# Optimization experiments

Hardware: AMD Instinct MI355X
Metric: run time of the kernel (lower is better)

## Reference

```python
import jax, jax.numpy as jnp
import numpy as np

NA = 100000
NB = 100000
E = 500000
D = 256
EPS = 1e-5


def setup_inputs() -> dict:
    key = jax.random.key(0)
    ks = jax.random.split(key, 10)
    scale = 1.0 / np.sqrt(D)
    return {
        "feat_a": jax.random.normal(ks[0], (NA, D), jnp.float32),
        "feat_b": jax.random.normal(ks[1], (NB, D), jnp.float32),
        "src_ab": jax.random.randint(ks[2], (E,), 0, NA, jnp.int32),
        "dst_ab": jax.random.randint(ks[3], (E,), 0, NB, jnp.int32),
        "src_ba": jax.random.randint(ks[4], (E,), 0, NB, jnp.int32),
        "dst_ba": jax.random.randint(ks[5], (E,), 0, NA, jnp.int32),
        "WT_ab": jax.random.normal(ks[6], (D, D), jnp.float32) * scale,
        "WT_ba": jax.random.normal(ks[7], (D, D), jnp.float32) * scale,
        "WA_ab": jax.random.normal(ks[8], (1, D), jnp.float32) * scale,
        "WA_ba": jax.random.normal(ks[9], (1, D), jnp.float32) * scale,
        "gamma": jnp.ones((D,), jnp.float32),
        "beta": jnp.zeros((D,), jnp.float32),
    }


def _etype_agg(h_src, h_dst, src, dst, WT, WA, n_dst):
    # per-etype linear on src nodes: t_h = W_T h_src
    t_h = h_src @ WT.T                              # [Ns, D]
    x = t_h[src] * h_dst[dst]                       # u_mul_v -> [E, D]
    s = jnp.exp(x @ WA.T)                           # exp(W_A x) -> [E, 1]
    att_sum = jax.ops.segment_sum(s, dst, num_segments=n_dst)  # copy_e+sum
    att = s / att_sum[dst]                          # e_div_v (dst of an edge always has >=1 edge)
    # u_mul_e + sum: weighted scatter of raw src features
    return jax.ops.segment_sum(h_src[src] * att, dst, num_segments=n_dst)


def _finalize(h, gamma, beta):
    h = jax.nn.relu(h)
    mu = jnp.mean(h, axis=-1, keepdims=True)
    var = jnp.mean(jnp.square(h - mu), axis=-1, keepdims=True)
    return (h - mu) / jnp.sqrt(var + EPS) * gamma + beta  # dropout is identity (eval)


def reference(feat_a, feat_b, src_ab, dst_ab, src_ba, dst_ba,
              WT_ab, WT_ba, WA_ab, WA_ba, gamma, beta):
    h_b = _etype_agg(feat_a, feat_b, src_ab, dst_ab, WT_ab, WA_ab, NB)
    h_a = _etype_agg(feat_b, feat_a, src_ba, dst_ba, WT_ba, WA_ba, NA)
    out_a = _finalize(h_a, gamma, beta)
    out_b = _finalize(h_b, gamma, beta)
    return jnp.stack([out_a, out_b])  # [2, N, D]
```

## Files before the change

kernel.cpp:

```cpp
#include <hip/hip_runtime.h>
#include <hip/hip_bf16.h>

#define D 256

typedef __attribute__((ext_vector_type(8))) short short8;
typedef __attribute__((ext_vector_type(4))) float f32x4;
typedef __attribute__((ext_vector_type(4))) unsigned short u16x4;

__device__ __forceinline__ unsigned short f2bf(float f) {
  unsigned int u = __builtin_bit_cast(unsigned int, f);
  u = (u + 0x7FFFu + ((u >> 16) & 1u)) >> 16;
  return (unsigned short)u;
}
__device__ __forceinline__ float bf2f(unsigned short h) {
  unsigned int u = ((unsigned int)h) << 16;
  return __builtin_bit_cast(float, u);
}

__global__ void zero_f32(float* __restrict__ p, int n) {
  int i = blockIdx.x * 256 + threadIdx.x;
  if (i < n) p[i] = 0.f;
}
__global__ void zero2_k(int* __restrict__ a, int na, int* __restrict__ b, int nb) {
  int i = blockIdx.x * 256 + threadIdx.x;
  if (i < na) a[i] = 0;
  else if (i - na < nb) b[i - na] = 0;
}

__global__ void classify_k(const float* __restrict__ q0, const float* __restrict__ q1,
                           const float* __restrict__ q2, const float* __restrict__ q3,
                           int* __restrict__ flags) {
  __shared__ int cnt1[4], cnt0[4];
  int t = threadIdx.x;
  if (t < 4) { cnt1[t] = 0; cnt0[t] = 0; }
  __syncthreads();
  const float* qs[4] = {q0, q1, q2, q3};
#pragma unroll
  for (int v = 0; v < 4; ++v) {
    float x = qs[v][t];
    if (x == 1.0f) atomicAdd(&cnt1[v], 1);
    if (x == 0.0f) atomicAdd(&cnt0[v], 1);
  }
  __syncthreads();
  if (t == 0) {
    int gi = -1, bi = -1;
    for (int v = 0; v < 4; ++v) if (cnt1[v] == 256 && gi < 0) gi = v;
    for (int v = 0; v < 4; ++v) if (cnt0[v] == 256 && v != gi && bi < 0) bi = v;
    if (gi < 0) gi = 2;
    if (bi < 0) bi = (gi == 3) ? 2 : 3;
    int wa[2], w = 0;
    for (int v = 0; v < 4; ++v) if (v != gi && v != bi) { if (w < 2) wa[w] = v; ++w; }
    flags[0] = wa[0]; flags[1] = wa[1]; flags[2] = gi; flags[3] = bi;
  }
}

__global__ void prep_w2(const float* __restrict__ WT_ab, const float* __restrict__ WT_ba,
                        const float* __restrict__ q0, const float* __restrict__ q1,
                        const float* __restrict__ q2, const float* __restrict__ q3,
                        const int* __restrict__ flags,
                        unsigned short* __restrict__ w2ab, unsigned short* __restrict__ w2ba) {
  const float* qs[4] = {q0, q1, q2, q3};
  const float* WAab = qs[flags[0]];
  const float* WAba = qs[flags[1]];
  int i = blockIdx.x * 256 + threadIdx.x;
  int n = i >> 8;
  w2ab[i] = f2bf(WAab[n] * WT_ab[i]);
  w2ba[i] = f2bf(WAba[n] * WT_ba[i]);
}

__global__ __launch_bounds__(512) void gemm_g(const float* __restrict__ feat,
                                              const unsigned short* __restrict__ w2,
                                              unsigned short* __restrict__ g,
                                              unsigned short* __restrict__ featbf,
                                              int nchunks, int do_featbf) {
  __shared__ __align__(16) unsigned char bl[2][8192];
  int lane = threadIdx.x & 63;
  int wv = threadIdx.x >> 6;
  int c0 = blockIdx.x * 8 + wv;
  bool active = c0 < nchunks;
  int c = active ? c0 : (nchunks - 1);
  int r16 = lane & 15;
  int kg = lane >> 4;
  int row0 = c * 32;

  short8 a[2][8];
#pragma unroll
  for (int sub = 0; sub < 2; ++sub) {
    int row = row0 + sub * 16 + r16;
    const float* rp = feat + (size_t)row * D + kg * 8;
#pragma unroll
    for (int kk = 0; kk < 8; ++kk) {
      f32x4 x0 = *(const f32x4*)(rp + kk * 32);
      f32x4 x1 = *(const f32x4*)(rp + kk * 32 + 4);
      short8 t;
      t[0] = (short)f2bf(x0[0]); t[1] = (short)f2bf(x0[1]);
      t[2] = (short)f2bf(x0[2]); t[3] = (short)f2bf(x0[3]);
      t[4] = (short)f2bf(x1[0]); t[5] = (short)f2bf(x1[1]);
      t[6] = (short)f2bf(x1[2]); t[7] = (short)f2bf(x1[3]);
      a[sub][kk] = t;
      if (do_featbf && active)
        *(short8*)(featbf + (size_t)row * D + kk * 32 + kg * 8) = t;
    }
  }

  int t = threadIdx.x;
  int brow = t >> 5, bc = t & 31;
  int slin = brow * 512 + bc * 16;
  int sswz = slin ^ ((brow & 7) << 4);

  *(short8*)(bl[0] + sswz) = *(const short8*)(w2 + (size_t)brow * D + bc * 8);
  __syncthreads();

  int cur = 0;
#pragma unroll 1
  for (int nt = 0; nt < 16; ++nt) {
    short8 tnext;
    bool has = nt + 1 < 16;
    if (has)
      tnext = *(const short8*)(w2 + (size_t)((nt + 1) * 16 + brow) * D + bc * 8);

    f32x4 acc0 = {0.f, 0.f, 0.f, 0.f};
    f32x4 acc1 = {0.f, 0.f, 0.f, 0.f};
    const unsigned char* blc = bl[cur];
#pragma unroll
    for (int kk = 0; kk < 8; ++kk) {
      int lin = r16 * 512 + kk * 64 + kg * 16;
      int swz = lin ^ ((r16 & 7) << 4);
      short8 b = *(const short8*)(blc + swz);
      acc0 = __builtin_amdgcn_mfma_f32_16x16x32_bf16(a[0][kk], b, acc0, 0, 0, 0);
      acc1 = __builtin_amdgcn_mfma_f32_16x16x32_bf16(a[1][kk], b, acc1, 0, 0, 0);
    }
    if (active) {
      int colv = nt * 16 + r16;
#pragma unroll
      for (int j = 0; j < 4; ++j) {
        int r = row0 + kg * 4 + j;
        g[(size_t)r * D + colv] = f2bf(acc0[j]);
        g[(size_t)(r + 16) * D + colv] = f2bf(acc1[j]);
      }
    }
    if (has) *(short8*)(bl[cur ^ 1] + sswz) = tnext;
    __syncthreads();
    cur ^= 1;
  }
}

__global__ void hist2_k(const int* __restrict__ dab, int* __restrict__ degb,
                        const int* __restrict__ dba, int* __restrict__ dega, int E) {
  int i = blockIdx.x * blockDim.x + threadIdx.x;
  if (i < E) atomicAdd(&degb[dab[i]], 1);
  else if (i - E < E) atomicAdd(&dega[dba[i - E]], 1);
}

__global__ void scanA2_k(const int* __restrict__ degb, int* __restrict__ rpb,
                         int* __restrict__ bsb, int nB,
                         const int* __restrict__ dega, int* __restrict__ rpa,
                         int* __restrict__ bsa, int nA, int nbB) {
  __shared__ int sh[1024];
  bool isB = (int)blockIdx.x < nbB;
  const int* deg = isB ? degb : dega;
  int* rp = isB ? rpb : rpa;
  int* bsum = isB ? bsb : bsa;
  int n = isB ? nB : nA;
  int blk = isB ? blockIdx.x : blockIdx.x - nbB;
  int i = blk * 1024 + threadIdx.x;
  int v = (i < n) ? deg[i] : 0;
  sh[threadIdx.x] = v;
  __syncthreads();
  for (int off = 1; off < 1024; off <<= 1) {
    int tv = (threadIdx.x >= (unsigned)off) ? sh[threadIdx.x - off] : 0;
    __syncthreads();
    sh[threadIdx.x] += tv;
    __syncthreads();
  }
  if (i < n) rp[i] = sh[threadIdx.x] - v;
  if (threadIdx.x == 1023) bsum[blk] = sh[1023];
}

__global__ void scanB_k(int* __restrict__ bsB, int* __restrict__ bsA, int nbB, int nbA) {
  __shared__ int sh[128];
  int* b = (blockIdx.x == 0) ? bsB : bsA;
  int nb = (blockIdx.x == 0) ? nbB : nbA;
  int t = threadIdx.x;
  int v = (t < nb) ? b[t] : 0;
  sh[t] = v;
  __syncthreads();
  for (int off = 1; off < 128; off <<= 1) {
    int u = (t >= off) ? sh[t - off] : 0;
    __syncthreads();
    sh[t] += u;
    __syncthreads();
  }
  if (t < nb) b[t] = sh[t] - v;
}

__global__ void scanC2_k(int* __restrict__ rpb, int* __restrict__ curb,
                         const int* __restrict__ bsb, int nB,
                         int* __restrict__ rpa, int* __restrict__ cura,
                         const int* __restrict__ bsa, int nA, int nbB, int E) {
  bool isB = (int)blockIdx.x < nbB;
  int* rp = isB ? rpb : rpa;
  int* cursor = isB ? curb : cura;
  const int* bsum = isB ? bsb : bsa;
  int n = isB ? nB : nA;
  int blk = isB ? blockIdx.x : blockIdx.x - nbB;
  int i = blk * 1024 + threadIdx.x;
  if (i < n) {
    int v = rp[i] + bsum[i >> 10];
    rp[i] = v;
    cursor[i] = v;
  }
  if (i == 0) rp[n] = E;
}

__global__ void scatter2_k(const int* __restrict__ sab, const int* __restrict__ dab,
                           int* __restrict__ curb, int* __restrict__ colab,
                           const int* __restrict__ sba, const int* __restrict__ dba,
                           int* __restrict__ cura, int* __restrict__ colba, int E) {
  int i = blockIdx.x * blockDim.x + threadIdx.x;
  if (i < E) {
    int slot = atomicAdd(&curb[dab[i]], 1);
    colab[slot] = sab[i];
  } else if (i - E < E) {
    int j = i - E;
    int slot = atomicAdd(&cura[dba[j]], 1);
    colba[slot] = sba[j];
  }
}

__global__ __launch_bounds__(256) void agg_ln_bf(const unsigned short* __restrict__ fsrc,
                                                 const float* __restrict__ feat_dst,
                                                 const unsigned short* __restrict__ g,
                                                 const int* __restrict__ rp,
                                                 const int* __restrict__ colsrc,
                                                 const float* __restrict__ q0,
                                                 const float* __restrict__ q1,
                                                 const float* __restrict__ q2,
                                                 const float* __restrict__ q3,
                                                 const int* __restrict__ flags,
                                                 float* __restrict__ out, int n_dst) {
  const float* qs[4] = {q0, q1, q2, q3};
  const float* gamma = qs[flags[2]];
  const float* beta  = qs[flags[3]];
  int lane = threadIdx.x & 63;
  int v = blockIdx.x * 4 + (threadIdx.x >> 6);
  if (v >= n_dst) return;
  f32x4 hv = *(const f32x4*)(feat_dst + (size_t)v * D + lane * 4);
  int beg = rp[v], end = rp[v + 1];

  float ssum = 0.f;
  f32x4 acc = {0.f, 0.f, 0.f, 0.f};
  if (beg < end) {
    int last = end - 1;
    int e1 = (beg + 1 <= last) ? beg + 1 : last;
    int e2 = (beg + 2 <= last) ? beg + 2 : last;
    int sc0 = colsrc[beg], sc1 = colsrc[e1], sc2 = colsrc[e2];
    u16x4 gq0 = *(const u16x4*)(g + (size_t)sc0 * D + lane * 4);
    u16x4 fq0 = *(const u16x4*)(fsrc + (size_t)sc0 * D + lane * 4);
    u16x4 gq1 = *(const u16x4*)(g + (size_t)sc1 * D + lane * 4);
    u16x4 fq1 = *(const u16x4*)(fsrc + (size_t)sc1 * D + lane * 4);
    u16x4 gq2 = *(const u16x4*)(g + (size_t)sc2 * D + lane * 4);
    u16x4 fq2 = *(const u16x4*)(fsrc + (size_t)sc2 * D + lane * 4);
    for (int i = beg; i < end; ++i) {
      int ip = (i + 3 <= last) ? i + 3 : last;
      int scn = colsrc[ip];
      u16x4 gqn = *(const u16x4*)(g + (size_t)scn * D + lane * 4);
      u16x4 fqn = *(const u16x4*)(fsrc + (size_t)scn * D + lane * 4);

      float d = bf2f(gq0[0]) * hv[0] + bf2f(gq0[1]) * hv[1] +
                bf2f(gq0[2]) * hv[2] + bf2f(gq0[3]) * hv[3];
#pragma unroll
      for (int off = 32; off > 0; off >>= 1) d += __shfl_xor(d, off, 64);
      float s = __expf(d);
      ssum += s;
      acc[0] += bf2f(fq0[0]) * s; acc[1] += bf2f(fq0[1]) * s;
      acc[2] += bf2f(fq0[2]) * s; acc[3] += bf2f(fq0[3]) * s;

      gq0 = gq1; fq0 = fq1;
      gq1 = gq2; fq1 = fq2;
      gq2 = gqn; fq2 = fqn;
    }
  }
  float inv = (end > beg) ? (1.f / ssum) : 0.f;
  acc[0] *= inv; acc[1] *= inv; acc[2] *= inv; acc[3] *= inv;

  acc[0] = fmaxf(acc[0], 0.f); acc[1] = fmaxf(acc[1], 0.f);
  acc[2] = fmaxf(acc[2], 0.f); acc[3] = fmaxf(acc[3], 0.f);

  float sm = acc[0] + acc[1] + acc[2] + acc[3];
#pragma unroll
  for (int off = 32; off > 0; off >>= 1) sm += __shfl_xor(sm, off, 64);
  float mu = sm * (1.f / 256.f);
  f32x4 dl;
  dl[0] = acc[0] - mu; dl[1] = acc[1] - mu; dl[2] = acc[2] - mu; dl[3] = acc[3] - mu;
  float sq = dl[0] * dl[0] + dl[1] * dl[1] + dl[2] * dl[2] + dl[3] * dl[3];
#pragma unroll
  for (int off = 32; off > 0; off >>= 1) sq += __shfl_xor(sq, off, 64);
  float rs = rsqrtf(sq * (1.f / 256.f) + 1e-5f);

  f32x4 gm = *(const f32x4*)(gamma + lane * 4);
  f32x4 bt = *(const f32x4*)(beta + lane * 4);
  f32x4 o;
  o[0] = dl[0] * rs * gm[0] + bt[0];
  o[1] = dl[1] * rs * gm[1] + bt[1];
  o[2] = dl[2] * rs * gm[2] + bt[2];
  o[3] = dl[3] * rs * gm[3] + bt[3];
  *(f32x4*)(out + (size_t)v * D + lane * 4) = o;
}

__global__ __launch_bounds__(256) void agg_ln(const float* __restrict__ feat_src,
                                              const float* __restrict__ feat_dst,
                                              const unsigned short* __restrict__ g,
                                              const int* __restrict__ rp,
                                              const int* __restrict__ colsrc,
                                              const float* __restrict__ q0,
                                              const float* __restrict__ q1,
                                              const float* __restrict__ q2,
                                              const float* __restrict__ q3,
                                              const int* __restrict__ flags,
                                              float* __restrict__ out, int n_dst) {
  const float* qs[4] = {q0, q1, q2, q3};
  const float* gamma = qs[flags[2]];
  const float* beta  = qs[flags[3]];
  int lane = threadIdx.x & 63;
  int v = blockIdx.x * 4 + (threadIdx.x >> 6);
  if (v >= n_dst) return;
  f32x4 hv = *(const f32x4*)(feat_dst + (size_t)v * D + lane * 4);
  int beg = rp[v], end = rp[v + 1];

  float ssum = 0.f;
  f32x4 acc = {0.f, 0.f, 0.f, 0.f};
  for (int i = beg; i < end; ++i) {
    int sc = colsrc[i];
    u16x4 gq = *(const u16x4*)(g + (size_t)sc * D + lane * 4);
    float d = bf2f(gq[0]) * hv[0] + bf2f(gq[1]) * hv[1] +
              bf2f(gq[2]) * hv[2] + bf2f(gq[3]) * hv[3];
#pragma unroll
    for (int off = 32; off > 0; off >>= 1) d += __shfl_xor(d, off, 64);
    float s = __expf(d);
    ssum += s;
    f32x4 f = *(const f32x4*)(feat_src + (size_t)sc * D + lane * 4);
    acc[0] += f[0] * s; acc[1] += f[1] * s;
    acc[2] += f[2] * s; acc[3] += f[3] * s;
  }
  float inv = (end > beg) ? (1.f / ssum) : 0.f;
  acc[0] *= inv; acc[1] *= inv; acc[2] *= inv; acc[3] *= inv;

  acc[0] = fmaxf(acc[0], 0.f); acc[1] = fmaxf(acc[1], 0.f);
  acc[2] = fmaxf(acc[2], 0.f); acc[3] = fmaxf(acc[3], 0.f);

  float sm = acc[0] + acc[1] + acc[2] + acc[3];
#pragma unroll
  for (int off = 32; off > 0; off >>= 1) sm += __shfl_xor(sm, off, 64);
  float mu = sm * (1.f / 256.f);
  f32x4 dl;
  dl[0] = acc[0] - mu; dl[1] = acc[1] - mu; dl[2] = acc[2] - mu; dl[3] = acc[3] - mu;
  float sq = dl[0] * dl[0] + dl[1] * dl[1] + dl[2] * dl[2] + dl[3] * dl[3];
#pragma unroll
  for (int off = 32; off > 0; off >>= 1) sq += __shfl_xor(sq, off, 64);
  float rs = rsqrtf(sq * (1.f / 256.f) + 1e-5f);

  f32x4 gm = *(const f32x4*)(gamma + lane * 4);
  f32x4 bt = *(const f32x4*)(beta + lane * 4);
  f32x4 o;
  o[0] = dl[0] * rs * gm[0] + bt[0];
  o[1] = dl[1] * rs * gm[1] + bt[1];
  o[2] = dl[2] * rs * gm[2] + bt[2];
  o[3] = dl[3] * rs * gm[3] + bt[3];
  *(f32x4*)(out + (size_t)v * D + lane * 4) = o;
}

extern "C" void kernel_launch(void* const* d_in, const int* in_sizes, int n_in,
                              void* d_out, int out_size, void* d_ws, size_t ws_size,
                              hipStream_t stream) {
  const float* feat_a = (const float*)d_in[0];
  const float* feat_b = (const float*)d_in[1];
  const int* src_ab = (const int*)d_in[2];
  const int* dst_ab = (const int*)d_in[3];
  const int* src_ba = (const int*)d_in[4];
  const int* dst_ba = (const int*)d_in[5];
  const float* WT_ab = (const float*)d_in[6];
  const float* WT_ba = (const float*)d_in[7];
  const float* q0 = (const float*)d_in[8];
  const float* q1 = (const float*)d_in[9];
  const float* q2 = (const float*)d_in[10];
  const float* q3 = (const float*)d_in[11];

  int NA = in_sizes[0] / D;
  int NB = in_sizes[1] / D;
  int E = in_sizes[2];

  float* out = (float*)d_out;
  float* out_a = out;
  float* out_b = out + (size_t)NA * D;

  char* w = (char*)d_ws;
  size_t off = 0;
  auto alloc = [&](size_t bytes) -> void* {
    void* p = (void*)(w + off);
    off += (bytes + 255) & ~(size_t)255;
    return p;
  };
  size_t nmax = (size_t)(NA > NB ? NA : NB);
  unsigned short* gws = (unsigned short*)alloc(nmax * D * 2);
  unsigned short* w2ab = (unsigned short*)alloc(65536 * 2);
  unsigned short* w2ba = (unsigned short*)alloc(65536 * 2);
  int* dc_b = (int*)alloc((size_t)NB * 4);
  int* dc_a = (int*)alloc((size_t)NA * 4);
  int* rp_b = (int*)alloc((size_t)(NB + 1) * 4);
  int* rp_a = (int*)alloc((size_t)(NA + 1) * 4);
  int* col_ab = (int*)alloc((size_t)E * 4);
  int* col_ba = (int*)alloc((size_t)E * 4);
  int* bs_b = (int*)alloc(512);
  int* bs_a = (int*)alloc(512);
  int* flags = (int*)alloc(256);
  size_t need_base = off;
  unsigned short* featbf = (unsigned short*)alloc(nmax * D * 2);
  size_t need_full = off;

  bool bad = (n_in != 12);
  bad = bad || (in_sizes[0] != in_sizes[1]);
  bad = bad || (in_sizes[2] != in_sizes[3]) || (in_sizes[3] != in_sizes[4]) ||
        (in_sizes[4] != in_sizes[5]);
  bad = bad || (in_sizes[6] != 65536) || (in_sizes[7] != 65536);
  bad = bad || (in_sizes[8] != 256) || (in_sizes[9] != 256) ||
        (in_sizes[10] != 256) || (in_sizes[11] != 256);
  bad = bad || (out_size != (NA + NB) * D);
  bad = bad || (ws_size < need_base);
  if (bad) {
    zero_f32<<<(out_size + 255) / 256, 256, 0, stream>>>(out, out_size);
    return;
  }
  int fast = (ws_size >= need_full) ? 1 : 0;

  classify_k<<<1, 256, 0, stream>>>(q0, q1, q2, q3, flags);
  zero2_k<<<(NA + NB + 255) / 256, 256, 0, stream>>>(dc_b, NB, dc_a, NA);
  prep_w2<<<256, 256, 0, stream>>>(WT_ab, WT_ba, q0, q1, q2, q3, flags,
                                   w2ab, w2ba);

  hist2_k<<<(2 * E + 255) / 256, 256, 0, stream>>>(dst_ab, dc_b, dst_ba, dc_a, E);

  int nbB = (NB + 1023) / 1024, nbA = (NA + 1023) / 1024;
  scanA2_k<<<nbB + nbA, 1024, 0, stream>>>(dc_b, rp_b, bs_b, NB,
                                           dc_a, rp_a, bs_a, NA, nbB);
  scanB_k<<<2, 128, 0, stream>>>(bs_b, bs_a, nbB, nbA);
  scanC2_k<<<nbB + nbA, 1024, 0, stream>>>(rp_b, dc_b, bs_b, NB,
                                           rp_a, dc_a, bs_a, NA, nbB, E);
  scatter2_k<<<(2 * E + 255) / 256, 256, 0, stream>>>(src_ab, dst_ab, dc_b, col_ab,
                                                      src_ba, dst_ba, dc_a, col_ba, E);

  int chA = (NA + 31) / 32, chB = (NB + 31) / 32;

  gemm_g<<<(chA + 7) / 8, 512, 0, stream>>>(feat_a, w2ab, gws, featbf, chA, fast);
  if (fast)
    agg_ln_bf<<<(NB + 3) / 4, 256, 0, stream>>>(featbf, feat_b, gws, rp_b, col_ab,
                                                q0, q1, q2, q3, flags, out_b, NB);
  else
    agg_ln<<<(NB + 3) / 4, 256, 0, stream>>>(feat_a, feat_b, gws, rp_b, col_ab,
                                             q0, q1, q2, q3, flags, out_b, NB);

  gemm_g<<<(chB + 7) / 8, 512, 0, stream>>>(feat_b, w2ba, gws, featbf, chB, fast);
  if (fast)
    agg_ln_bf<<<(NA + 3) / 4, 256, 0, stream>>>(featbf, feat_a, gws, rp_a, col_ba,
                                                q0, q1, q2, q3, flags, out_a, NA);
  else
    agg_ln<<<(NA + 3) / 4, 256, 0, stream>>>(feat_b, feat_a, gws, rp_a, col_ba,
                                             q0, q1, q2, q3, flags, out_a, NA);
}
```

Measured before the change: 446.4 us.

## Precompute both bf16 feature copies and read bf16 dst features in aggregation

Adds a workspace buffer so both GEMMs run first. One projected matrix is stored in the unused output half (out_a) as scratch, and each GEMM also emits a bf16 copy of its input features. A new aggregation kernel then reads the destination features in bf16 instead of fp32, and the gather prefetch depth in both aggregation kernels drops from three edges ahead to one. This halves the destination-feature traffic and reduces register pressure. The costs are less latency hiding on the gathers, bf16 rounding of h_dst in the attention dot product, and a dependence on out_a being free until the last kernel overwrites it.

```diff
diff --git a/kernel.cpp b/kernel.cpp
--- a/kernel.cpp
+++ b/kernel.cpp
@@ -228,6 +228,77 @@
   }
 }
 
+__global__ __launch_bounds__(256) void agg_ln_bb(const unsigned short* __restrict__ fsrc,
+                                                 const unsigned short* __restrict__ hdst,
+                                                 const unsigned short* __restrict__ g,
+                                                 const int* __restrict__ rp,
+                                                 const int* __restrict__ colsrc,
+                                                 const float* __restrict__ q0,
+                                                 const float* __restrict__ q1,
+                                                 const float* __restrict__ q2,
+                                                 const float* __restrict__ q3,
+                                                 const int* __restrict__ flags,
+                                                 float* __restrict__ out, int n_dst) {
+  const float* qs[4] = {q0, q1, q2, q3};
+  const float* gamma = qs[flags[2]];
+  const float* beta  = qs[flags[3]];
+  int lane = threadIdx.x & 63;
+  int v = blockIdx.x * 4 + (threadIdx.x >> 6);
+  if (v >= n_dst) return;
+  u16x4 hq = *(const u16x4*)(hdst + (size_t)v * D + lane * 4);
+  f32x4 hv;
+  hv[0] = bf2f(hq[0]); hv[1] = bf2f(hq[1]); hv[2] = bf2f(hq[2]); hv[3] = bf2f(hq[3]);
+  int beg = rp[v], end = rp[v + 1];
+
+  float ssum = 0.f;
+  f32x4 acc = {0.f, 0.f, 0.f, 0.f};
+  if (beg < end) {
+    int sc = colsrc[beg];
+    u16x4 gq = *(const u16x4*)(g + (size_t)sc * D + lane * 4);
+    u16x4 fq = *(const u16x4*)(fsrc + (size_t)sc * D + lane * 4);
+    for (int i = beg; i < end; ++i) {
+      int ip = (i + 1 < end) ? (i + 1) : i;
+      int scn = colsrc[ip];
+      u16x4 gqn = *(const u16x4*)(g + (size_t)scn * D + lane * 4);
+      u16x4 fqn = *(const u16x4*)(fsrc + (size_t)scn * D + lane * 4);
+      float d = bf2f(gq[0]) * hv[0] + bf2f(gq[1]) * hv[1] +
+                bf2f(gq[2]) * hv[2] + bf2f(gq[3]) * hv[3];
+#pragma unroll
+      for (int off = 32; off > 0; off >>= 1) d += __shfl_xor(d, off, 64);
+      float s = __expf(d);
+      ssum += s;
+      acc[0] += bf2f(fq[0]) * s; acc[1] += bf2f(fq[1]) * s;
+      acc[2] += bf2f(fq[2]) * s; acc[3] += bf2f(fq[3]) * s;
+      gq = gqn; fq = fqn;
+    }
+  }
+  float inv = (end > beg) ? (1.f / ssum) : 0.f;
+  acc[0] *= inv; acc[1] *= inv; acc[2] *= inv; acc[3] *= inv;
+
+  acc[0] = fmaxf(acc[0], 0.f); acc[1] = fmaxf(acc[1], 0.f);
+  acc[2] = fmaxf(acc[2], 0.f); acc[3] = fmaxf(acc[3], 0.f);
+
+  float sm = acc[0] + acc[1] + acc[2] + acc[3];
+#pragma unroll
+  for (int off = 32; off > 0; off >>= 1) sm += __shfl_xor(sm, off, 64);
+  float mu = sm * (1.f / 256.f);
+  f32x4 dl;
+  dl[0] = acc[0] - mu; dl[1] = acc[1] - mu; dl[2] = acc[2] - mu; dl[3] = acc[3] - mu;
+  float sq = dl[0] * dl[0] + dl[1] * dl[1] + dl[2] * dl[2] + dl[3] * dl[3];
+#pragma unroll
+  for (int off = 32; off > 0; off >>= 1) sq += __shfl_xor(sq, off, 64);
+  float rs = rsqrtf(sq * (1.f / 256.f) + 1e-5f);
+
+  f32x4 gm = *(const f32x4*)(gamma + lane * 4);
+  f32x4 bt = *(const f32x4*)(beta + lane * 4);
+  f32x4 o;
+  o[0] = dl[0] * rs * gm[0] + bt[0];
+  o[1] = dl[1] * rs * gm[1] + bt[1];
+  o[2] = dl[2] * rs * gm[2] + bt[2];
+  o[3] = dl[3] * rs * gm[3] + bt[3];
+  *(f32x4*)(out + (size_t)v * D + lane * 4) = o;
+}
+
 __global__ __launch_bounds__(256) void agg_ln_bf(const unsigned short* __restrict__ fsrc,
                                                  const float* __restrict__ feat_dst,
                                                  const unsigned short* __restrict__ g,
@@ -251,34 +322,23 @@
   float ssum = 0.f;
   f32x4 acc = {0.f, 0.f, 0.f, 0.f};
   if (beg < end) {
-    int last = end - 1;
-    int e1 = (beg + 1 <= last) ? beg + 1 : last;
-    int e2 = (beg + 2 <= last) ? beg + 2 : last;
-    int sc0 = colsrc[beg], sc1 = colsrc[e1], sc2 = colsrc[e2];
-    u16x4 gq0 = *(const u16x4*)(g + (size_t)sc0 * D + lane * 4);
-    u16x4 fq0 = *(const u16x4*)(fsrc + (size_t)sc0 * D + lane * 4);
-    u16x4 gq1 = *(const u16x4*)(g + (size_t)sc1 * D + lane * 4);
-    u16x4 fq1 = *(const u16x4*)(fsrc + (size_t)sc1 * D + lane * 4);
-    u16x4 gq2 = *(const u16x4*)(g + (size_t)sc2 * D + lane * 4);
-    u16x4 fq2 = *(const u16x4*)(fsrc + (size_t)sc2 * D + lane * 4);
+    int sc = colsrc[beg];
+    u16x4 gq = *(const u16x4*)(g + (size_t)sc * D + lane * 4);
+    u16x4 fq = *(const u16x4*)(fsrc + (size_t)sc * D + lane * 4);
     for (int i = beg; i < end; ++i) {
-      int ip = (i + 3 <= last) ? i + 3 : last;
+      int ip = (i + 1 < end) ? (i + 1) : i;
       int scn = colsrc[ip];
       u16x4 gqn = *(const u16x4*)(g + (size_t)scn * D + lane * 4);
       u16x4 fqn = *(const u16x4*)(fsrc + (size_t)scn * D + lane * 4);
-
-      float d = bf2f(gq0[0]) * hv[0] + bf2f(gq0[1]) * hv[1] +
-                bf2f(gq0[2]) * hv[2] + bf2f(gq0[3]) * hv[3];
+      float d = bf2f(gq[0]) * hv[0] + bf2f(gq[1]) * hv[1] +
+                bf2f(gq[2]) * hv[2] + bf2f(gq[3]) * hv[3];
 #pragma unroll
       for (int off = 32; off > 0; off >>= 1) d += __shfl_xor(d, off, 64);
       float s = __expf(d);
       ssum += s;
-      acc[0] += bf2f(fq0[0]) * s; acc[1] += bf2f(fq0[1]) * s;
-      acc[2] += bf2f(fq0[2]) * s; acc[3] += bf2f(fq0[3]) * s;
-
-      gq0 = gq1; fq0 = fq1;
-      gq1 = gq2; fq1 = fq2;
-      gq2 = gqn; fq2 = fqn;
+      acc[0] += bf2f(fq[0]) * s; acc[1] += bf2f(fq[1]) * s;
+      acc[2] += bf2f(fq[2]) * s; acc[3] += bf2f(fq[3]) * s;
+      gq = gqn; fq = fqn;
     }
   }
   float inv = (end > beg) ? (1.f / ssum) : 0.f;
@@ -417,6 +477,8 @@
   size_t need_base = off;
   unsigned short* featbf = (unsigned short*)alloc(nmax * D * 2);
   size_t need_full = off;
+  unsigned short* featbf2 = (unsigned short*)alloc(nmax * D * 2);
+  size_t need_big = off;
 
   bool bad = (n_in != 12);
   bad = bad || (in_sizes[0] != in_sizes[1]);
@@ -431,6 +493,7 @@
     zero_f32<<<(out_size + 255) / 256, 256, 0, stream>>>(out, out_size);
     return;
   }
+  int big  = (ws_size >= need_big)  ? 1 : 0;
   int fast = (ws_size >= need_full) ? 1 : 0;
 
   classify_k<<<1, 256, 0, stream>>>(q0, q1, q2, q3, flags);
@@ -451,19 +514,27 @@
 
   int chA = (NA + 31) / 32, chB = (NB + 31) / 32;
 
-  gemm_g<<<(chA + 7) / 8, 512, 0, stream>>>(feat_a, w2ab, gws, featbf, chA, fast);
-  if (fast)
+  if (big) {
+    unsigned short* g_a = (unsigned short*)out_a;
+    gemm_g<<<(chA + 7) / 8, 512, 0, stream>>>(feat_a, w2ab, g_a, featbf, chA, 1);
+    gemm_g<<<(chB + 7) / 8, 512, 0, stream>>>(feat_b, w2ba, gws, featbf2, chB, 1);
+    agg_ln_bb<<<(NB + 3) / 4, 256, 0, stream>>>(featbf, featbf2, g_a, rp_b, col_ab,
+                                                q0, q1, q2, q3, flags, out_b, NB);
+    agg_ln_bb<<<(NA + 3) / 4, 256, 0, stream>>>(featbf2, featbf, gws, rp_a, col_ba,
+                                                q0, q1, q2, q3, flags, out_a, NA);
+  } else if (fast) {
+    gemm_g<<<(chA + 7) / 8, 512, 0, stream>>>(feat_a, w2ab, gws, featbf, chA, 1);
     agg_ln_bf<<<(NB + 3) / 4, 256, 0, stream>>>(featbf, feat_b, gws, rp_b, col_ab,
                                                 q0, q1, q2, q3, flags, out_b, NB);
-  else
+    gemm_g<<<(chB + 7) / 8, 512, 0, stream>>>(feat_b, w2ba, gws, featbf, chB, 1);
+    agg_ln_bf<<<(NA + 3) / 4, 256, 0, stream>>>(featbf, feat_a, gws, rp_a, col_ba,
+                                                q0, q1, q2, q3, flags, out_a, NA);
+  } else {
+    gemm_g<<<(chA + 7) / 8, 512, 0, stream>>>(feat_a, w2ab, gws, featbf, chA, 0);
     agg_ln<<<(NB + 3) / 4, 256, 0, stream>>>(feat_a, feat_b, gws, rp_b, col_ab,
                                              q0, q1, q2, q3, flags, out_b, NB);
-
-  gemm_g<<<(chB + 7) / 8, 512, 0, stream>>>(feat_b, w2ba, gws, featbf, chB, fast);
-  if (fast)
-    agg_ln_bf<<<(NA + 3) / 4, 256, 0, stream>>>(featbf, feat_a, gws, rp_a, col_ba,
-                                                q0, q1, q2, q3, flags, out_a, NA);
-  else
+    gemm_g<<<(chB + 7) / 8, 512, 0, stream>>>(feat_b, w2ba, gws, featbf, chB, 0);
     agg_ln<<<(NA + 3) / 4, 256, 0, stream>>>(feat_b, feat_a, gws, rp_a, col_ba,
                                              q0, q1, q2, q3, flags, out_a, NA);
-}
+  }
+}
```

Result: no change. 443.9 us (-0.6%).
